# Optimization experiments

Measured on AMD Instinct MI355X. Metric: run time of the kernel, lower is better.

The kernel has to match this reference:

```python
import jax, jax.numpy as jnp
import numpy as np

IGNORE_INDEX = -100
BETA = 0.1
VOCAB = 32000
HIDDEN = 4096
TWO_B = 8   # concatenated [chosen; rejected]
SEQ = 512


def setup_inputs() -> dict:
    key = jax.random.key(0)
    k1, k2, k3, k4, k5 = jax.random.split(key, 5)
    lin_weight = jax.random.normal(k1, (VOCAB, HIDDEN), dtype=jnp.float32) * 0.02
    _input = jax.random.normal(k2, (TWO_B, SEQ, HIDDEN), dtype=jnp.float32)
    target = jax.random.randint(k3, (TWO_B, SEQ), 0, VOCAB, dtype=jnp.int64)
    ref_chosen_logps = jax.random.normal(k4, (TWO_B // 2,), dtype=jnp.float32)
    ref_rejected_logps = jax.random.normal(k5, (TWO_B // 2,), dtype=jnp.float32)
    bias = jnp.zeros((VOCAB,), dtype=jnp.float32)
    return {"lin_weight": lin_weight, "_input": _input, "target": target,
            "ref_chosen_logps": ref_chosen_logps, "ref_rejected_logps": ref_rejected_logps,
            "bias": bias}


def reference(lin_weight, _input, target, ref_chosen_logps, ref_rejected_logps, bias):
    B2 = target.shape[0]
    len_chosen = B2 // 2
    # fused linear + log-softmax (materialized here; the kernel chunks this)
    logits = jnp.einsum("bth,vh->btv", _input, lin_weight) + bias  # [2B, T, V]
    logp = jax.nn.log_softmax(logits, axis=-1)
    mask = (target != IGNORE_INDEX)
    safe_tgt = jnp.where(mask, target, 0)
    per_tok = jnp.take_along_axis(logp, safe_tgt[..., None], axis=-1)[..., 0]
    per_tok = jnp.where(mask, per_tok, 0.0)                         # [2B, T]
    cnt = mask.sum(axis=-1).astype(per_tok.dtype)                   # tokens per sequence
    avg_logps = per_tok.sum(axis=-1) / cnt                          # average logp per sequence
    chosen_logps = avg_logps[:len_chosen]
    rejected_logps = avg_logps[len_chosen:]
    # NLL loss on chosen half, normalized by chosen non-ignored token count
    nll_loss = -per_tok[:len_chosen].sum() / mask[:len_chosen].sum().astype(per_tok.dtype)
    # DPO preference loss
    chosen_adv = chosen_logps - ref_chosen_logps
    rejected_adv = rejected_logps - ref_rejected_logps
    pref_logits = BETA * (chosen_adv - rejected_adv)
    pref_loss = -jnp.mean(jax.nn.log_sigmoid(pref_logits))
    return pref_loss + nll_loss
```

## Files before the change

### kernel.cpp

```cpp
#include <hip/hip_runtime.h>
#include <hip/hip_bf16.h>
#include <stdint.h>

#define M_TOK 4096
#define NV    32000
#define KH    4096
#define KTILES 64
#define IGNORE_INDEX (-100)

#define BM    128
#define BN    128
#define BK    64
#define NBLK_OLD  (NV / BN)
#define MBLK_OLD  (M_TOK / BM)

typedef __bf16 bf16;
typedef bf16  bf16x8 __attribute__((ext_vector_type(8)));
typedef bf16  bf16x4 __attribute__((ext_vector_type(4)));
typedef float f32x4  __attribute__((ext_vector_type(4)));

__device__ __forceinline__ void async_copy16(const void* g, void* l) {
    __builtin_amdgcn_global_load_lds(
        (const __attribute__((address_space(1))) void*)g,
        (__attribute__((address_space(3))) void*)l, 16, 0, 0);
}

__global__ __launch_bounds__(256) void cvt_bf16_kernel(const float* __restrict__ src,
                                                       bf16* __restrict__ dst, int n4) {
    int i = blockIdx.x * blockDim.x + threadIdx.x;
    int stride = gridDim.x * blockDim.x;
    const float4* s4 = (const float4*)src;
    bf16x4* d4 = (bf16x4*)dst;
    for (; i < n4; i += stride) {
        float4 v = s4[i];
        bf16x4 o;
        o[0] = (bf16)v.x; o[1] = (bf16)v.y; o[2] = (bf16)v.z; o[3] = (bf16)v.w;
        d4[i] = o;
    }
}

__global__ __launch_bounds__(256) void tlogit_kernel(const float* __restrict__ inp,
                                                     const float* __restrict__ W,
                                                     const float* __restrict__ bias,
                                                     const int* __restrict__ target,
                                                     float* __restrict__ tlogit) {
    const int wave = threadIdx.x >> 6, lane = threadIdx.x & 63;
    const int t = blockIdx.x * 4 + wave;
    if (t >= M_TOK) return;
    int tg = target[t];
    int row = (tg == IGNORE_INDEX) ? 0 : tg;
    const float4* a4 = (const float4*)(inp + (long)t * KH);
    const float4* w4 = (const float4*)(W + (long)row * KH);
    float acc = 0.f;
#pragma unroll
    for (int i = 0; i < 16; i++) {
        float4 a = a4[i * 64 + lane];
        float4 w = w4[i * 64 + lane];
        acc += a.x * w.x + a.y * w.y + a.z * w.z + a.w * w.w;
    }
#pragma unroll
    for (int d = 1; d < 64; d <<= 1) acc += __shfl_xor(acc, d, 64);
    if (lane == 0) tlogit[t] = acc + bias[row];
}

__global__ __launch_bounds__(512, 2) void gemm_lse256_kernel(
    const bf16* __restrict__ A, const bf16* __restrict__ W16,
    const float* __restrict__ bias, float* __restrict__ pm, float* __restrict__ ps)
{
    __shared__ __align__(16) char smem[131072];
    const int tid = threadIdx.x;
    const int lane = tid & 63;
    const int wid = tid >> 6;
    const int wm = wid >> 2, wn = wid & 3;

    const int bx = blockIdx.x;
    const int wg = (bx & 7) * 250 + (bx >> 3);
    const int nblk = wg >> 4;
    const int mblk = wg & 15;
    const int m0 = mblk << 8;
    const int n0 = nblk << 8;

    const int srow = tid >> 3, slot = tid & 7;
    const int chunk = slot ^ (srow & 7);
    const bf16* aSrc = A   + (size_t)(m0 + srow) * KH + chunk * 8;
    const bf16* bSrc = W16 + (size_t)(n0 + srow) * KH + chunk * 8;
    char* dA0 = smem +      0 + tid * 16;
    char* dB0 = smem +  32768 + tid * 16;
    char* dA1 = smem +  65536 + tid * 16;
    char* dB1 = smem +  98304 + tid * 16;

#define STG_A(DST, h, tt) do { if ((tt) < KTILES) {                            \
        const bf16* _s = aSrc + (size_t)(h) * 128 * KH + (size_t)(tt) * 64;    \
        async_copy16(_s,                   (DST) + (h) * 16384);               \
        async_copy16(_s + (size_t)64 * KH, (DST) + (h) * 16384 + 8192); } } while (0)
#define STG_B(DST, h, tt) do { if ((tt) < KTILES) {                            \
        const bf16* _s = bSrc + (size_t)(h) * 128 * KH + (size_t)(tt) * 64;    \
        async_copy16(_s,                   (DST) + (h) * 16384);               \
        async_copy16(_s + (size_t)64 * KH, (DST) + (h) * 16384 + 8192); } } while (0)

    const int rA = wm * 128 + (lane & 15);
    const int rB = wn * 64  + (lane & 15);
    const int co0 = ((((lane >> 4) + 0) ^ (lane & 7)) << 3);
    const int co1 = ((((lane >> 4) + 4) ^ (lane & 7)) << 3);

    const bf16* sA[2] = { (const bf16*)(smem),         (const bf16*)(smem + 65536) };
    const bf16* sB[2] = { (const bf16*)(smem + 32768), (const bf16*)(smem + 98304) };

    f32x4 acc[8][4] = {};
    bf16x8 regA[8], regB0[4], regB1[4];

#define MFMA_Q(MB, NB, BR)                                                      \
    _Pragma("unroll")                                                           \
    for (int mt = 0; mt < 4; ++mt)                                              \
        _Pragma("unroll")                                                       \
        for (int nt = 0; nt < 2; ++nt)                                          \
            _Pragma("unroll")                                                   \
            for (int ks = 0; ks < 2; ++ks)                                      \
                acc[(MB) + mt][(NB) + nt] = __builtin_amdgcn_mfma_f32_16x16x32_bf16( \
                    regA[mt * 2 + ks], BR[nt * 2 + ks], acc[(MB) + mt][(NB) + nt], 0, 0, 0);

#define TILE_BODY(b, t, DA_O, DB_C, DA_C) do {                                  \
                                                      \
    _Pragma("unroll") for (int mt = 0; mt < 4; ++mt) {                          \
        regA[mt * 2]     = *(const bf16x8*)(sA[b] + (rA + mt * 16) * 64 + co0); \
        regA[mt * 2 + 1] = *(const bf16x8*)(sA[b] + (rA + mt * 16) * 64 + co1); } \
    _Pragma("unroll") for (int nt = 0; nt < 2; ++nt) {                          \
        regB0[nt * 2]     = *(const bf16x8*)(sB[b] + (rB + nt * 16) * 64 + co0); \
        regB0[nt * 2 + 1] = *(const bf16x8*)(sB[b] + (rB + nt * 16) * 64 + co1); } \
    STG_A(DA_O, 1, (t) + 1);                                                    \
    __builtin_amdgcn_s_barrier();                                               \
    asm volatile("s_waitcnt lgkmcnt(0)" ::: "memory");                          \
    __builtin_amdgcn_sched_barrier(0);                                          \
    __builtin_amdgcn_s_setprio(1);                                              \
    MFMA_Q(0, 0, regB0)                                                         \
    __builtin_amdgcn_s_setprio(0);                                              \
    __builtin_amdgcn_s_barrier();                                               \
                                                      \
    _Pragma("unroll") for (int nt = 0; nt < 2; ++nt) {                          \
        regB1[nt * 2]     = *(const bf16x8*)(sB[b] + (rB + (nt + 2) * 16) * 64 + co0); \
        regB1[nt * 2 + 1] = *(const bf16x8*)(sB[b] + (rB + (nt + 2) * 16) * 64 + co1); } \
    __builtin_amdgcn_s_barrier();                                               \
    asm volatile("s_waitcnt lgkmcnt(0)" ::: "memory");                          \
    __builtin_amdgcn_sched_barrier(0);                                          \
    __builtin_amdgcn_s_setprio(1);                                              \
    MFMA_Q(0, 2, regB1)                                                         \
    __builtin_amdgcn_s_setprio(0);                                              \
    __builtin_amdgcn_s_barrier();                                               \
                                                      \
    _Pragma("unroll") for (int mt = 0; mt < 4; ++mt) {                          \
        regA[mt * 2]     = *(const bf16x8*)(sA[b] + (rA + (mt + 4) * 16) * 64 + co0); \
        regA[mt * 2 + 1] = *(const bf16x8*)(sA[b] + (rA + (mt + 4) * 16) * 64 + co1); } \
    STG_B(DB_C, 0, (t) + 2);                                                    \
    __builtin_amdgcn_s_barrier();                                               \
    asm volatile("s_waitcnt lgkmcnt(0)" ::: "memory");                          \
    __builtin_amdgcn_sched_barrier(0);                                          \
    __builtin_amdgcn_s_setprio(1);                                              \
    MFMA_Q(4, 2, regB1)                                                         \
    __builtin_amdgcn_s_setprio(0);                                              \
    __builtin_amdgcn_s_barrier();                                               \
                                                      \
    STG_B(DB_C, 1, (t) + 2);                                                    \
    STG_A(DA_C, 0, (t) + 2);                                                    \
    __builtin_amdgcn_s_barrier();                                               \
    __builtin_amdgcn_s_setprio(1);                                              \
    MFMA_Q(4, 0, regB0)                                                         \
    __builtin_amdgcn_s_setprio(0);                                              \
    if ((t) + 2 < KTILES) { asm volatile("s_waitcnt vmcnt(6)" ::: "memory"); }  \
    else                  { asm volatile("s_waitcnt vmcnt(0)" ::: "memory"); }  \
    __builtin_amdgcn_s_barrier();                                               \
} while (0)

    STG_A(dA0, 0, 0); STG_A(dA0, 1, 0);
    STG_B(dB0, 0, 0); STG_B(dB0, 1, 0);
    STG_B(dB1, 0, 1); STG_B(dB1, 1, 1);
    STG_A(dA1, 0, 1);
    asm volatile("s_waitcnt vmcnt(6)" ::: "memory");
    __builtin_amdgcn_s_barrier();

#pragma unroll 1
    for (int t = 0; t < KTILES; t += 2) {
        TILE_BODY(0, t,     dA1, dB0, dA0);
        TILE_BODY(1, t + 1, dA0, dB1, dA1);
    }

    float bv[4];
#pragma unroll
    for (int nt = 0; nt < 4; ++nt)
        bv[nt] = bias[n0 + wn * 64 + nt * 16 + (lane & 15)];

    float (*red_m)[256] = (float (*)[256])(smem);
    float (*red_s)[256] = (float (*)[256])(smem + 4096);

#pragma unroll
    for (int mt = 0; mt < 8; ++mt) {
        float rm[4], rs[4];
#pragma unroll
        for (int r = 0; r < 4; ++r) {
            float v0 = acc[mt][0][r] + bv[0];
            float v1 = acc[mt][1][r] + bv[1];
            float v2 = acc[mt][2][r] + bv[2];
            float v3 = acc[mt][3][r] + bv[3];
            float mx = fmaxf(fmaxf(v0, v1), fmaxf(v2, v3));
#pragma unroll
            for (int d = 1; d < 16; d <<= 1) mx = fmaxf(mx, __shfl_xor(mx, d, 64));
            float s = __expf(v0 - mx) + __expf(v1 - mx) + __expf(v2 - mx) + __expf(v3 - mx);
#pragma unroll
            for (int d = 1; d < 16; d <<= 1) s += __shfl_xor(s, d, 64);
            rm[r] = mx; rs[r] = s;
        }
        if ((lane & 15) == 0) {
            int rl = wm * 128 + mt * 16 + (lane >> 4) * 4;
#pragma unroll
            for (int r = 0; r < 4; ++r) {
                red_m[wn][rl + r] = rm[r];
                red_s[wn][rl + r] = rs[r];
            }
        }
    }
    __syncthreads();
    if (tid < 256) {
        float mm = red_m[0][tid], ss = red_s[0][tid];
#pragma unroll
        for (int j = 1; j < 4; ++j) {
            float mj = red_m[j][tid], sj = red_s[j][tid];
            float m2 = fmaxf(mm, mj);
            ss = ss * __expf(mm - m2) + sj * __expf(mj - m2);
            mm = m2;
        }
        size_t idx = (size_t)nblk * M_TOK + m0 + tid;
        pm[idx] = mm;
        ps[idx] = ss;
    }
#undef TILE_BODY
#undef MFMA_Q
#undef STG_A
#undef STG_B
}

template<bool PRECONV>
__global__ __launch_bounds__(256) void gemm_lse_kernel(const bf16* __restrict__ A,
                                                       const void* __restrict__ Wv,
                                                       const float* __restrict__ bias,
                                                       float* __restrict__ pm,
                                                       float* __restrict__ ps) {
    const int tid = threadIdx.x;
    const int wave = tid >> 6, lane = tid & 63;
    const int wm = wave & 1, wn = wave >> 1;
    const int bx = blockIdx.x;
    const int mblk = bx & 31;
    const int nblk = bx >> 5;
    const int m0 = mblk * BM, n0 = nblk * BN;

    __shared__ bf16 sA[BM * BK];
    __shared__ bf16 sB[BN * BK];
    __shared__ float red_m[2][BM];
    __shared__ float red_s[2][BM];

    f32x4 acc[4][4] = {};

    const int srow  = tid >> 3;
    const int slot  = tid & 7;
    const int chunk = slot ^ (srow & 7);
    const bf16* aptr = A + (long)(m0 + srow) * KH + chunk * 8;
    bf16* sA_dst = sA + tid * 8;
    bf16* sB_dst = sB + tid * 8;

    const bf16*  Wb = (const bf16*)Wv;
    const float* Wf = (const float*)Wv;
    const bf16*  bptr16 = Wb + (long)(n0 + srow) * KH + chunk * 8;
    const float* bptr32 = Wf + (long)(n0 + srow) * KH + chunk * 8;

    for (int k0 = 0; k0 < KH; k0 += BK) {
#pragma unroll
        for (int i = 0; i < 4; i++)
            async_copy16(aptr + (long)i * 32 * KH + k0, sA_dst + i * 2048);
        if (PRECONV) {
#pragma unroll
            for (int i = 0; i < 4; i++)
                async_copy16(bptr16 + (long)i * 32 * KH + k0, sB_dst + i * 2048);
        } else {
#pragma unroll
            for (int i = 0; i < 4; i++) {
                const float* wp = bptr32 + (long)i * 32 * KH + k0;
                float4 w0 = *(const float4*)(wp);
                float4 w1 = *(const float4*)(wp + 4);
                bf16x8 b;
                b[0] = (bf16)w0.x; b[1] = (bf16)w0.y; b[2] = (bf16)w0.z; b[3] = (bf16)w0.w;
                b[4] = (bf16)w1.x; b[5] = (bf16)w1.y; b[6] = (bf16)w1.z; b[7] = (bf16)w1.w;
                *(bf16x8*)(sB + (i * 32 + srow) * BK + slot * 8) = b;
            }
        }
        __syncthreads();
#pragma unroll
        for (int kk = 0; kk < BK; kk += 32) {
            bf16x8 af[4], bfr[4];
            const int rbase = wm * 64 + (lane & 15);
            const int cbase = wn * 64 + (lane & 15);
            const int c = (kk >> 3) + (lane >> 4);
            const int xoff = ((c ^ (lane & 7)) << 3);
#pragma unroll
            for (int t = 0; t < 4; t++)
                af[t] = *(const bf16x8*)(sA + (rbase + t * 16) * BK + xoff);
#pragma unroll
            for (int t = 0; t < 4; t++)
                bfr[t] = *(const bf16x8*)(sB + (cbase + t * 16) * BK + xoff);
#pragma unroll
            for (int mt = 0; mt < 4; mt++)
#pragma unroll
                for (int nt = 0; nt < 4; nt++)
                    acc[mt][nt] = __builtin_amdgcn_mfma_f32_16x16x32_bf16(
                        af[mt], bfr[nt], acc[mt][nt], 0, 0, 0);
        }
        __syncthreads();
    }

    float bv[4];
#pragma unroll
    for (int nt = 0; nt < 4; nt++)
        bv[nt] = bias[n0 + wn * 64 + nt * 16 + (lane & 15)];

#pragma unroll
    for (int mt = 0; mt < 4; mt++) {
        float rm[4], rs[4];
#pragma unroll
        for (int r = 0; r < 4; r++) {
            float v0 = acc[mt][0][r] + bv[0];
            float v1 = acc[mt][1][r] + bv[1];
            float v2 = acc[mt][2][r] + bv[2];
            float v3 = acc[mt][3][r] + bv[3];
            float mx = fmaxf(fmaxf(v0, v1), fmaxf(v2, v3));
#pragma unroll
            for (int d = 1; d < 16; d <<= 1) mx = fmaxf(mx, __shfl_xor(mx, d, 64));
            float s = __expf(v0 - mx) + __expf(v1 - mx) + __expf(v2 - mx) + __expf(v3 - mx);
#pragma unroll
            for (int d = 1; d < 16; d <<= 1) s += __shfl_xor(s, d, 64);
            rm[r] = mx; rs[r] = s;
        }
        if ((lane & 15) == 0) {
            int rl = wm * 64 + mt * 16 + (lane >> 4) * 4;
#pragma unroll
            for (int r = 0; r < 4; r++) {
                red_m[wn][rl + r] = rm[r];
                red_s[wn][rl + r] = rs[r];
            }
        }
    }
    __syncthreads();
    if (tid < BM) {
        float m0v = red_m[0][tid], s0v = red_s[0][tid];
        float m1v = red_m[1][tid], s1v = red_s[1][tid];
        float mm = fmaxf(m0v, m1v);
        float ss = s0v * __expf(m0v - mm) + s1v * __expf(m1v - mm);
        long idx = (long)nblk * M_TOK + m0 + tid;
        pm[idx] = mm;
        ps[idx] = ss;
    }
}

__global__ __launch_bounds__(256) void lse_combine_kernel(const float* __restrict__ pm,
                                                          const float* __restrict__ ps,
                                                          const float* __restrict__ tlogit,
                                                          const int* __restrict__ target,
                                                          float* __restrict__ per_tok,
                                                          int nblkN) {
    int t = blockIdx.x * blockDim.x + threadIdx.x;
    if (t >= M_TOK) return;
    float m = -1e30f, s = 0.f;
    for (int j = 0; j < nblkN; j++) {
        float mj = pm[j * M_TOK + t];
        float sj = ps[j * M_TOK + t];
        if (mj > m) {
            s = s * expf(m - mj) + sj;
            m = mj;
        } else {
            s += sj * expf(mj - m);
        }
    }
    float lse = m + logf(s);
    int tg = target[t];
    per_tok[t] = (tg != IGNORE_INDEX) ? (tlogit[t] - lse) : 0.0f;
}

__global__ __launch_bounds__(512) void final_kernel(const float* __restrict__ per_tok,
                                                    const int* __restrict__ target,
                                                    const float* __restrict__ refc,
                                                    const float* __restrict__ refr,
                                                    float* __restrict__ out) {
    __shared__ float ssum[8];
    __shared__ float scnt[8];
    const int w = threadIdx.x >> 6, lane = threadIdx.x & 63;
    float sum = 0.f, cnt = 0.f;
#pragma unroll
    for (int i = 0; i < 8; i++) {
        int t = w * 512 + i * 64 + lane;
        sum += per_tok[t];
        cnt += (target[t] != IGNORE_INDEX) ? 1.f : 0.f;
    }
#pragma unroll
    for (int d = 1; d < 64; d <<= 1) {
        sum += __shfl_xor(sum, d, 64);
        cnt += __shfl_xor(cnt, d, 64);
    }
    if (lane == 0) { ssum[w] = sum; scnt[w] = cnt; }
    __syncthreads();
    if (threadIdx.x == 0) {
        float avg[8];
#pragma unroll
        for (int i = 0; i < 8; i++) avg[i] = ssum[i] / scnt[i];
        float nll_num = 0.f, nll_den = 0.f;
#pragma unroll
        for (int i = 0; i < 4; i++) { nll_num += ssum[i]; nll_den += scnt[i]; }
        float nll = -nll_num / nll_den;
        float pref = 0.f;
#pragma unroll
        for (int i = 0; i < 4; i++) {
            float x = 0.1f * ((avg[i] - refc[i]) - (avg[i + 4] - refr[i]));
            float ls = (x >= 0.f) ? -log1pf(expf(-x)) : (x - log1pf(expf(x)));
            pref += -ls;
        }
        pref *= 0.25f;
        out[0] = pref + nll;
    }
}

extern "C" void kernel_launch(void* const* d_in, const int* in_sizes, int n_in,
                              void* d_out, int out_size, void* d_ws, size_t ws_size,
                              hipStream_t stream) {
    const float* W    = (const float*)d_in[0];
    const float* inp  = (const float*)d_in[1];
    const int*   tgt  = (const int*)d_in[2];
    const float* refc = (const float*)d_in[3];
    const float* refr = (const float*)d_in[4];
    const float* bias = (const float*)d_in[5];
    float* out = (float*)d_out;

    char* ws = (char*)d_ws;
    size_t off = 0;
    bf16* A16 = (bf16*)(ws + off); off += (size_t)M_TOK * KH * sizeof(bf16);
    float* pm = (float*)(ws + off); off += (size_t)NBLK_OLD * M_TOK * sizeof(float);
    float* ps = (float*)(ws + off); off += (size_t)NBLK_OLD * M_TOK * sizeof(float);
    float* tl = (float*)(ws + off); off += (size_t)M_TOK * sizeof(float);
    float* ptk = (float*)(ws + off); off += (size_t)M_TOK * sizeof(float);
    bf16* W16 = (bf16*)(ws + off);
    size_t need = off + (size_t)NV * KH * sizeof(bf16);

    cvt_bf16_kernel<<<4096, 256, 0, stream>>>(inp, A16, (M_TOK * KH) / 4);
    tlogit_kernel<<<M_TOK / 4, 256, 0, stream>>>(inp, W, bias, tgt, tl);
    if (ws_size >= need) {
        cvt_bf16_kernel<<<16384, 256, 0, stream>>>(W, W16, (int)(((size_t)NV * KH) / 4));
        gemm_lse256_kernel<<<16 * 125, 512, 0, stream>>>(A16, W16, bias, pm, ps);
        lse_combine_kernel<<<(M_TOK + 255) / 256, 256, 0, stream>>>(pm, ps, tl, tgt, ptk, 125);
    } else {
        gemm_lse_kernel<false><<<MBLK_OLD * NBLK_OLD, 256, 0, stream>>>(A16, (const void*)W, bias, pm, ps);
        lse_combine_kernel<<<(M_TOK + 255) / 256, 256, 0, stream>>>(pm, ps, tl, tgt, ptk, NBLK_OLD);
    }
    final_kernel<<<1, 512, 0, stream>>>(ptk, tgt, refc, refr, out);
}
```

Before: 1.714 ms.

## Restructure GEMM main loop to prefetch next tile fragments and split A/B staging

Reworks the 256x256 GEMM k-loop so LDS fragment loads for the next k-tile are issued during the current tile's last MFMA quadrant. It uses double register buffers for A and B fragments and partial lgkmcnt waits instead of full drains. A-tile global-to-LDS staging now loads all four row groups at once, one tile ahead, and the vmcnt thresholds are adjusted to match. The aim is to hide LDS read latency behind MFMAs, at the cost of more VGPR pressure and a tighter ordering of buffer reuse that could cause races.

```diff
diff --git a/kernel.cpp b/kernel.cpp
--- a/kernel.cpp
+++ b/kernel.cpp
@@ -89,11 +89,13 @@
     char* dA1 = smem +  65536 + tid * 16;
     char* dB1 = smem +  98304 + tid * 16;
 
-#define STG_A(DST, h, tt) do { if ((tt) < KTILES) {                            \
-        const bf16* _s = aSrc + (size_t)(h) * 128 * KH + (size_t)(tt) * 64;    \
-        async_copy16(_s,                   (DST) + (h) * 16384);               \
-        async_copy16(_s + (size_t)64 * KH, (DST) + (h) * 16384 + 8192); } } while (0)
-#define STG_B(DST, h, tt) do { if ((tt) < KTILES) {                            \
+#define STG_A4(DST, tt) do { if ((tt) < KTILES) {                              \
+        const bf16* _s = aSrc + (size_t)(tt) * 64;                             \
+        async_copy16(_s,                    (DST));                            \
+        async_copy16(_s + (size_t)64  * KH, (DST) + 8192);                     \
+        async_copy16(_s + (size_t)128 * KH, (DST) + 16384);                    \
+        async_copy16(_s + (size_t)192 * KH, (DST) + 24576); } } while (0)
+#define STG_BH(DST, h, tt) do { if ((tt) < KTILES) {                           \
         const bf16* _s = bSrc + (size_t)(h) * 128 * KH + (size_t)(tt) * 64;    \
         async_copy16(_s,                   (DST) + (h) * 16384);               \
         async_copy16(_s + (size_t)64 * KH, (DST) + (h) * 16384 + 8192); } } while (0)
@@ -106,81 +108,95 @@
     const bf16* sA[2] = { (const bf16*)(smem),         (const bf16*)(smem + 65536) };
     const bf16* sB[2] = { (const bf16*)(smem + 32768), (const bf16*)(smem + 98304) };
 
+#define LDA(BUF, mt, ks) (*(const bf16x8*)(sA[(BUF)] + (rA + (mt) * 16) * 64 + ((ks) ? co1 : co0)))
+#define LDB(BUF, nt, ks) (*(const bf16x8*)(sB[(BUF)] + (rB + (nt) * 16) * 64 + ((ks) ? co1 : co0)))
+
     f32x4 acc[8][4] = {};
-    bf16x8 regA[8], regB0[4], regB1[4];
-
-#define MFMA_Q(MB, NB, BR)                                                      \
+    bf16x8 rA0[8], rA1[8], rB_0[4], rB_1[4];
+
+#define MFMA_Q(MB, NB, AR, BR)                                                  \
     _Pragma("unroll")                                                           \
-    for (int mt = 0; mt < 4; ++mt)                                              \
+    for (int ks = 0; ks < 2; ++ks)                                              \
         _Pragma("unroll")                                                       \
-        for (int nt = 0; nt < 2; ++nt)                                          \
+        for (int mt = 0; mt < 4; ++mt)                                          \
             _Pragma("unroll")                                                   \
-            for (int ks = 0; ks < 2; ++ks)                                      \
+            for (int nt = 0; nt < 2; ++nt)                                      \
                 acc[(MB) + mt][(NB) + nt] = __builtin_amdgcn_mfma_f32_16x16x32_bf16( \
-                    regA[mt * 2 + ks], BR[nt * 2 + ks], acc[(MB) + mt][(NB) + nt], 0, 0, 0);
-
-#define TILE_BODY(b, t, DA_O, DB_C, DA_C) do {                                  \
-                                                      \
-    _Pragma("unroll") for (int mt = 0; mt < 4; ++mt) {                          \
-        regA[mt * 2]     = *(const bf16x8*)(sA[b] + (rA + mt * 16) * 64 + co0); \
-        regA[mt * 2 + 1] = *(const bf16x8*)(sA[b] + (rA + mt * 16) * 64 + co1); } \
-    _Pragma("unroll") for (int nt = 0; nt < 2; ++nt) {                          \
-        regB0[nt * 2]     = *(const bf16x8*)(sB[b] + (rB + nt * 16) * 64 + co0); \
-        regB0[nt * 2 + 1] = *(const bf16x8*)(sB[b] + (rB + nt * 16) * 64 + co1); } \
-    STG_A(DA_O, 1, (t) + 1);                                                    \
+                    AR[mt * 2 + ks], BR[nt * 2 + ks], acc[(MB) + mt][(NB) + nt], 0, 0, 0);
+
+#define TILE_BODY(b, t, RBC, RBN, DA_O, DB_C) do {                              \
+               \
+    _Pragma("unroll") for (int nt = 0; nt < 2; ++nt)                            \
+        _Pragma("unroll") for (int ks = 0; ks < 2; ++ks)                        \
+            RBN[nt * 2 + ks] = LDB(b, nt + 2, ks);                              \
+    STG_A4(DA_O, (t) + 1);                                                      \
+    __builtin_amdgcn_s_barrier();                                               \
+    asm volatile("s_waitcnt lgkmcnt(4)" ::: "memory");                          \
+    __builtin_amdgcn_sched_barrier(0);                                          \
+    __builtin_amdgcn_s_setprio(1);                                              \
+    MFMA_Q(0, 0, rA0, RBC)                                                      \
+    __builtin_amdgcn_s_setprio(0);                                              \
+    __builtin_amdgcn_s_barrier();                                               \
+                           \
+    _Pragma("unroll") for (int mt = 0; mt < 4; ++mt)                            \
+        _Pragma("unroll") for (int ks = 0; ks < 2; ++ks)                        \
+            rA1[mt * 2 + ks] = LDA(b, mt + 4, ks);                              \
+    __builtin_amdgcn_s_barrier();                                               \
+    asm volatile("s_waitcnt lgkmcnt(8)" ::: "memory");                          \
+    __builtin_amdgcn_sched_barrier(0);                                          \
+    __builtin_amdgcn_s_setprio(1);                                              \
+    MFMA_Q(0, 2, rA0, RBN)                                                      \
+    __builtin_amdgcn_s_setprio(0);                                              \
+    __builtin_amdgcn_s_barrier();                                               \
+              \
+    STG_BH(DB_C, 0, (t) + 2);                                                   \
     __builtin_amdgcn_s_barrier();                                               \
     asm volatile("s_waitcnt lgkmcnt(0)" ::: "memory");                          \
     __builtin_amdgcn_sched_barrier(0);                                          \
     __builtin_amdgcn_s_setprio(1);                                              \
-    MFMA_Q(0, 0, regB0)                                                         \
+    MFMA_Q(4, 2, rA1, RBN)                                                      \
     __builtin_amdgcn_s_setprio(0);                                              \
-    __builtin_amdgcn_s_barrier();                                               \
-                                                      \
-    _Pragma("unroll") for (int nt = 0; nt < 2; ++nt) {                          \
-        regB1[nt * 2]     = *(const bf16x8*)(sB[b] + (rB + (nt + 2) * 16) * 64 + co0); \
-        regB1[nt * 2 + 1] = *(const bf16x8*)(sB[b] + (rB + (nt + 2) * 16) * 64 + co1); } \
-    __builtin_amdgcn_s_barrier();                                               \
-    asm volatile("s_waitcnt lgkmcnt(0)" ::: "memory");                          \
+    if ((t) + 2 < KTILES) { asm volatile("s_waitcnt vmcnt(2)" ::: "memory"); }  \
+    else                  { asm volatile("s_waitcnt vmcnt(0)" ::: "memory"); }  \
+    __builtin_amdgcn_s_barrier();                                               \
+                                               \
+    if ((t) + 1 < KTILES) {                                                     \
+        _Pragma("unroll") for (int mt = 0; mt < 4; ++mt)                        \
+            _Pragma("unroll") for (int ks = 0; ks < 2; ++ks)                    \
+                rA0[mt * 2 + ks] = LDA((b) ^ 1, mt, ks);                        \
+        _Pragma("unroll") for (int nt = 0; nt < 2; ++nt)                        \
+            _Pragma("unroll") for (int ks = 0; ks < 2; ++ks)                    \
+                RBN[nt * 2 + ks] = LDB((b) ^ 1, nt, ks);                        \
+    }                                                                           \
+    STG_BH(DB_C, 1, (t) + 2);                                                   \
+    __builtin_amdgcn_s_barrier();                                               \
     __builtin_amdgcn_sched_barrier(0);                                          \
     __builtin_amdgcn_s_setprio(1);                                              \
-    MFMA_Q(0, 2, regB1)                                                         \
+    MFMA_Q(4, 0, rA1, RBC)                                                      \
     __builtin_amdgcn_s_setprio(0);                                              \
     __builtin_amdgcn_s_barrier();                                               \
-                                                      \
-    _Pragma("unroll") for (int mt = 0; mt < 4; ++mt) {                          \
-        regA[mt * 2]     = *(const bf16x8*)(sA[b] + (rA + (mt + 4) * 16) * 64 + co0); \
-        regA[mt * 2 + 1] = *(const bf16x8*)(sA[b] + (rA + (mt + 4) * 16) * 64 + co1); } \
-    STG_B(DB_C, 0, (t) + 2);                                                    \
-    __builtin_amdgcn_s_barrier();                                               \
-    asm volatile("s_waitcnt lgkmcnt(0)" ::: "memory");                          \
-    __builtin_amdgcn_sched_barrier(0);                                          \
-    __builtin_amdgcn_s_setprio(1);                                              \
-    MFMA_Q(4, 2, regB1)                                                         \
-    __builtin_amdgcn_s_setprio(0);                                              \
-    __builtin_amdgcn_s_barrier();                                               \
-                                                      \
-    STG_B(DB_C, 1, (t) + 2);                                                    \
-    STG_A(DA_C, 0, (t) + 2);                                                    \
-    __builtin_amdgcn_s_barrier();                                               \
-    __builtin_amdgcn_s_setprio(1);                                              \
-    MFMA_Q(4, 0, regB0)                                                         \
-    __builtin_amdgcn_s_setprio(0);                                              \
-    if ((t) + 2 < KTILES) { asm volatile("s_waitcnt vmcnt(6)" ::: "memory"); }  \
-    else                  { asm volatile("s_waitcnt vmcnt(0)" ::: "memory"); }  \
-    __builtin_amdgcn_s_barrier();                                               \
 } while (0)
 
-    STG_A(dA0, 0, 0); STG_A(dA0, 1, 0);
-    STG_B(dB0, 0, 0); STG_B(dB0, 1, 0);
-    STG_B(dB1, 0, 1); STG_B(dB1, 1, 1);
-    STG_A(dA1, 0, 1);
-    asm volatile("s_waitcnt vmcnt(6)" ::: "memory");
+    STG_A4(dA0, 0);
+    STG_BH(dB0, 0, 0); STG_BH(dB0, 1, 0);
+    STG_BH(dB1, 0, 1); STG_BH(dB1, 1, 1);
+    asm volatile("s_waitcnt vmcnt(4)" ::: "memory");
     __builtin_amdgcn_s_barrier();
+#pragma unroll
+    for (int mt = 0; mt < 4; ++mt)
+#pragma unroll
+        for (int ks = 0; ks < 2; ++ks)
+            rA0[mt * 2 + ks] = LDA(0, mt, ks);
+#pragma unroll
+    for (int nt = 0; nt < 2; ++nt)
+#pragma unroll
+        for (int ks = 0; ks < 2; ++ks)
+            rB_0[nt * 2 + ks] = LDB(0, nt, ks);
 
 #pragma unroll 1
     for (int t = 0; t < KTILES; t += 2) {
-        TILE_BODY(0, t,     dA1, dB0, dA0);
-        TILE_BODY(1, t + 1, dA0, dB1, dA1);
+        TILE_BODY(0, t,     rB_0, rB_1, dA1, dB0);
+        TILE_BODY(1, t + 1, rB_1, rB_0, dA0, dB1);
     }
 
     float bv[4];
@@ -233,8 +249,10 @@
     }
 #undef TILE_BODY
 #undef MFMA_Q
-#undef STG_A
-#undef STG_B
+#undef LDA
+#undef LDB
+#undef STG_A4
+#undef STG_BH
 }
 
 template<bool PRECONV>
```

Result: slower. 2.251 ms (+31.4%).
